# Optimization experiments

Measured on AMD Instinct MI355X. Metric: run time of the kernel, lower is better.

## Reference

```python
import jax, jax.numpy as jnp
import numpy as np

N_SA_ITERS = 3
MESH_LR = 5.0
MESH_ITERS = 4
SH_ITERS = 5
EPS = 1e-8
B, N, D, S, H = 16, 16384, 64, 7, 128


def layer_norm(x, g, b):
    m = jnp.mean(x, -1, keepdims=True)
    v = jnp.var(x, -1, keepdims=True)
    return (x - m) * jax.lax.rsqrt(v + 1e-5) * g + b


def cdist(k, q):
    # k: [b,n,d], q: [b,s,d] -> euclidean distances [b,n,s]
    k2 = jnp.sum(k * k, -1)[:, :, None]
    q2 = jnp.sum(q * q, -1)[:, None, :]
    sq = k2 + q2 - 2.0 * jnp.einsum('bnd,bsd->bns', k, q)
    return jnp.sqrt(jnp.maximum(sq, 0.0) + 1e-12)


def sinkhorn(C, log_a, log_b, u, v, n_iters=SH_ITERS):
    # log-domain Sinkhorn. C: [b,n,s], log_a: [b,n], log_b: [b,s]
    p = -C
    for _ in range(n_iters):
        u = log_a - jax.nn.logsumexp(p + v[:, None, :], axis=2)
        v = log_b - jax.nn.logsumexp(p + u[:, :, None], axis=1)
    T = jnp.exp(p + u[:, :, None] + v[:, None, :])
    return T, u, v


def minimize_entropy_of_sinkhorn(C, log_a, log_b, mesh_lr=MESH_LR, n_mesh_iters=MESH_ITERS):
    # MESH: gradient descent on transport-plan entropy wrt the cost matrix,
    # warm-starting the sinkhorn duals across mesh iterations.
    u = jnp.zeros_like(log_a)
    v = jnp.zeros_like(log_b)
    for _ in range(n_mesh_iters):
        def ent(Cc, uu, vv):
            T, u2, v2 = sinkhorn(Cc, log_a, log_b, uu, vv)
            e = -jnp.sum(T * jnp.log(T + EPS))
            return e, (u2, v2)
        (_, (u, v)), g = jax.value_and_grad(ent, has_aux=True)(
            C, jax.lax.stop_gradient(u), jax.lax.stop_gradient(v))
        C = C - mesh_lr * g
    return C, u, v


def gru_cell(x, h, W_ih, W_hh, b_ih, b_hh):
    # PyTorch nn.GRUCell semantics
    gi = x @ W_ih.T + b_ih
    gh = h @ W_hh.T + b_hh
    i_r, i_z, i_n = jnp.split(gi, 3, axis=-1)
    h_r, h_z, h_n = jnp.split(gh, 3, axis=-1)
    r = jax.nn.sigmoid(i_r + h_r)
    z = jax.nn.sigmoid(i_z + h_z)
    n = jnp.tanh(i_n + r * h_n)
    return (1.0 - z) * n + z * h


def setup_inputs() -> dict:
    key = jax.random.key(0)
    ks = jax.random.split(key, 24)
    w = lambda k, shape, s=0.05: (jax.random.normal(k, shape, dtype=jnp.float32) * s)
    return {
        'inputs': jax.random.normal(ks[0], (B, N, D), dtype=jnp.float32),
        'slots_init': jax.random.normal(ks[1], (B, S, D), dtype=jnp.float32),
        'slots_mu': w(ks[2], (1, 1, D), 0.1),
        'slots_log_sigma': w(ks[3], (1, 1, D), 0.1),
        'Wq': w(ks[4], (D, D)), 'Wk': w(ks[5], (D, D)), 'Wv': w(ks[6], (D, D)),
        'gru_Wih': w(ks[7], (3 * D, D)), 'gru_Whh': w(ks[8], (3 * D, D)),
        'gru_bih': jnp.zeros((3 * D,), jnp.float32), 'gru_bhh': jnp.zeros((3 * D,), jnp.float32),
        'fc1_W': w(ks[9], (H, D)), 'fc1_b': jnp.zeros((H,), jnp.float32),
        'fc2_W': w(ks[10], (D, H)), 'fc2_b': jnp.zeros((D,), jnp.float32),
        'ln_in_g': jnp.ones((D,), jnp.float32), 'ln_in_b': jnp.zeros((D,), jnp.float32),
        'ln_sl_g': jnp.ones((D,), jnp.float32), 'ln_sl_b': jnp.zeros((D,), jnp.float32),
        'ln_ff_g': jnp.ones((D,), jnp.float32), 'ln_ff_b': jnp.zeros((D,), jnp.float32),
        'wi_W': w(ks[11], (1, D)), 'wi_b': jnp.zeros((1,), jnp.float32),
        'ws_W': w(ks[12], (1, D)), 'ws_b': jnp.zeros((1,), jnp.float32),
    }


def reference(inputs, slots_init, slots_mu, slots_log_sigma, Wq, Wk, Wv,
              gru_Wih, gru_Whh, gru_bih, gru_bhh, fc1_W, fc1_b, fc2_W, fc2_b,
              ln_in_g, ln_in_b, ln_sl_g, ln_sl_b, ln_ff_g, ln_ff_b,
              wi_W, wi_b, ws_W, ws_b):
    b_s, n_in, d = inputs.shape
    n_s = slots_init.shape[1]
    slots = slots_mu + jnp.exp(slots_log_sigma) * slots_init
    x = layer_norm(inputs, ln_in_g, ln_in_b)
    k = x @ Wk.T
    v = x @ Wv.T
    # input marginal a (sums to n_s over the n_in axis)
    a = jax.nn.softmax((x @ wi_W.T + wi_b)[..., 0], axis=-1) * n_s
    log_a = jnp.log(a)
    attn = None
    for _ in range(N_SA_ITERS):
        slots_prev = slots
        s_n = layer_norm(slots, ln_sl_g, ln_sl_b)
        b_marg = jax.nn.softmax((s_n @ ws_W.T + ws_b)[..., 0], axis=-1) * n_s
        log_b = jnp.log(b_marg)
        q = s_n @ Wq.T
        C = cdist(k, q)                                   # [b, n_in, n_s]
        C, p_u, q_v = minimize_entropy_of_sinkhorn(C, log_a, log_b)
        attn, _, _ = sinkhorn(C, log_a, log_b, p_u, q_v)  # [b, n_in, n_s]
        attn = jnp.transpose(attn, (0, 2, 1))             # [b, n_s, n_in]
        updates = jnp.matmul(attn, v)                     # [b, n_s, d]
        slots = gru_cell(updates.reshape(b_s * n_s, d), slots_prev.reshape(b_s * n_s, d),
                         gru_Wih, gru_Whh, gru_bih, gru_bhh).reshape(b_s, n_s, d)
        ff = jax.nn.relu(layer_norm(slots, ln_ff_g, ln_ff_b) @ fc1_W.T + fc1_b) @ fc2_W.T + fc2_b
        slots = slots + ff
    return slots, attn
```

## Files before the change

### kernel.cpp

```cpp
#include <hip/hip_runtime.h>
#include <math.h>

#define AGENTS __HIP_MEMORY_SCOPE_AGENT
typedef unsigned long long u64x;

constexpr int   CB   = 16;
constexpr int   CN   = 16384;
constexpr float LOG7 = 1.9459101090932196f;
constexpr float EPST = 1e-8f;

constexpr size_t ST1 = 0;
constexpr size_t ST2 = 1024;
constexpr size_t ST3 = 5120;
constexpr size_t NST = 234496;

constexpr size_t OFF_WQT = 468992;
constexpr size_t OFF_WIH = 473088;
constexpr size_t OFF_WHH = 485376;
constexpr size_t OFF_F1T = 497664;
constexpr size_t OFF_F2T = 505856;
constexpr size_t OFF_K   = 514048;
constexpr size_t OFF_V   = OFF_K + (size_t)CB * CN * 64;

__device__ __forceinline__ u64x pkf(float v, unsigned e) {
  return ((u64x)e << 32) | (u64x)__float_as_uint(v);
}
__device__ __forceinline__ void st_rlx(u64x* p, u64x v) {
  __hip_atomic_store(p, v, __ATOMIC_RELAXED, AGENTS);
}
__device__ __forceinline__ u64x ld_rlx(const u64x* p) {
  return __hip_atomic_load(const_cast<u64x*>(p), __ATOMIC_RELAXED, AGENTS);
}
__device__ __forceinline__ float poll_f(const u64x* p, unsigned e) {
  u64x q;
  do { q = ld_rlx(p); } while ((unsigned)(q >> 32) != e);
  return __uint_as_float((unsigned)q);
}
__device__ __forceinline__ float wsum64(float v) {
#pragma unroll
  for (int m = 1; m < 64; m <<= 1) v += __shfl_xor(v, m, 64);
  return v;
}
__device__ __forceinline__ float dot4(float4 a, float4 b) {
  return a.x * b.x + a.y * b.y + a.z * b.z + a.w * b.w;
}

__global__ void prep_kernel(const float* __restrict__ Wq, const float* __restrict__ Wih,
                            const float* __restrict__ Whh, const float* __restrict__ f1,
                            const float* __restrict__ f2, float* __restrict__ w) {
  size_t idx = blockIdx.x * blockDim.x + threadIdx.x;
  size_t stride = (size_t)gridDim.x * blockDim.x;
  u64x* st = reinterpret_cast<u64x*>(w);
  for (size_t i = idx; i < NST; i += stride) st_rlx(st + i, 0ULL);
  for (size_t i = idx; i < 64 * 64; i += stride) {
    int d = i / 64, j = i % 64;
    w[OFF_WQT + j * 64 + d] = Wq[d * 64 + j];
  }
  for (size_t i = idx; i < 192 * 64; i += stride) {
    int o = i / 64, j = i % 64;
    w[OFF_WIH + j * 192 + o] = Wih[o * 64 + j];
    w[OFF_WHH + j * 192 + o] = Whh[o * 64 + j];
  }
  for (size_t i = idx; i < 128 * 64; i += stride) {
    int o = i / 64, j = i % 64;
    w[OFF_F1T + j * 128 + o] = f1[o * 64 + j];
  }
  for (size_t i = idx; i < 64 * 128; i += stride) {
    int d = i / 128, j = i % 128;
    w[OFF_F2T + j * 64 + d] = f2[d * 128 + j];
  }
}

__launch_bounds__(1024, 4)
__global__ void slot_attn_kernel(
    const float* __restrict__ inputs, const float* __restrict__ sinit,
    const float* __restrict__ smu, const float* __restrict__ slsig,
    const float* __restrict__ Wk, const float* __restrict__ Wv,
    const float* __restrict__ gbih, const float* __restrict__ gbhh,
    const float* __restrict__ fc1b, const float* __restrict__ fc2b,
    const float* __restrict__ lin_g, const float* __restrict__ lin_b,
    const float* __restrict__ lsl_g, const float* __restrict__ lsl_b,
    const float* __restrict__ lff_g, const float* __restrict__ lff_b,
    const float* __restrict__ wi_W, const float* __restrict__ wi_b,
    const float* __restrict__ wsW, const float* __restrict__ wsB,
    float* __restrict__ out, float* __restrict__ w) {
  __shared__ float s_slots[448];
  __shared__ float s_snl[448];
  __shared__ float s_q[448];
  __shared__ float s_scr1[1344];
  __shared__ float s_scr2[1344];
  __shared__ float s_updl[448];
  __shared__ float s_T[8192];
  __shared__ float s_pupd[7168];
  __shared__ float s_z[48];
  __shared__ float s_eb[8];
  __shared__ float s_rb[8];
  __shared__ float s_gvl[8];
  __shared__ float s_q2[8];
  __shared__ float s_wl[8];
  __shared__ float s_redw[128];
  __shared__ float s_gath[128];
  __shared__ float s_misc[4];

  const int tid = threadIdx.x;
  const int lane = tid & 63, wid = tid >> 6;
  const int bb = blockIdx.x & 15;
  const int ib16 = blockIdx.x >> 4;
  const size_t grow = (size_t)bb * CN + ib16 * 1024 + tid;
  u64x* st = reinterpret_cast<u64x*>(w);
  float lg;

  {
    const float* xin = inputs + grow * 64;
    float4 xa[16];
#pragma unroll
    for (int c = 0; c < 16; ++c) xa[c] = reinterpret_cast<const float4*>(xin)[c];
    float s1 = 0;
#pragma unroll
    for (int c = 0; c < 16; ++c) s1 += xa[c].x + xa[c].y + xa[c].z + xa[c].w;
    float mn = s1 * (1.f / 64.f);
    float s2 = 0;
#pragma unroll
    for (int c = 0; c < 16; ++c) {
      float dx = xa[c].x - mn, dy = xa[c].y - mn, dz = xa[c].z - mn, dw = xa[c].w - mn;
      s2 += dx * dx + dy * dy + dz * dz + dw * dw;
    }
    float rs = rsqrtf(s2 * (1.f / 64.f) + 1e-5f);
#pragma unroll
    for (int c = 0; c < 16; ++c) {
      float4 g4 = reinterpret_cast<const float4*>(lin_g)[c];
      float4 b4 = reinterpret_cast<const float4*>(lin_b)[c];
      xa[c].x = (xa[c].x - mn) * rs * g4.x + b4.x;
      xa[c].y = (xa[c].y - mn) * rs * g4.y + b4.y;
      xa[c].z = (xa[c].z - mn) * rs * g4.z + b4.z;
      xa[c].w = (xa[c].w - mn) * rs * g4.w + b4.w;
    }
    lg = wi_b[0];
#pragma unroll
    for (int c = 0; c < 16; ++c) lg += dot4(xa[c], reinterpret_cast<const float4*>(wi_W)[c]);
#pragma unroll 1
    for (int half = 0; half < 2; ++half) {
      const float* W = half ? Wv : Wk;
      float* ob = w + (half ? OFF_V : OFF_K) + grow * 64;
#pragma unroll 1
      for (int oc = 0; oc < 8; ++oc) {
        float acc[8] = {0, 0, 0, 0, 0, 0, 0, 0};
#pragma unroll
        for (int c = 0; c < 16; ++c) {
          float4 xv = xa[c];
#pragma unroll
          for (int o8 = 0; o8 < 8; ++o8) {
            float4 w4 = reinterpret_cast<const float4*>(W + (size_t)(oc * 8 + o8) * 64)[c];
            acc[o8] += dot4(xv, w4);
          }
        }
        reinterpret_cast<float4*>(ob + oc * 8)[0] = make_float4(acc[0], acc[1], acc[2], acc[3]);
        reinterpret_cast<float4*>(ob + oc * 8)[1] = make_float4(acc[4], acc[5], acc[6], acc[7]);
      }
    }
    float mx = lg;
#pragma unroll
    for (int m = 1; m < 64; m <<= 1) mx = fmaxf(mx, __shfl_xor(mx, m, 64));
    float se = wsum64(__expf(lg - mx));
    if (lane == 0) { s_redw[wid * 8 + 0] = mx; s_redw[wid * 8 + 1] = se; }
    __syncthreads();
    if (wid == 0) {
      float m0 = (lane < 16) ? s_redw[lane * 8 + 0] : -1e30f;
      float e0 = (lane < 16) ? s_redw[lane * 8 + 1] : 0.f;
#pragma unroll
      for (int mm = 1; mm < 16; mm <<= 1) {
        float m1 = __shfl_xor(m0, mm, 64), e1 = __shfl_xor(e0, mm, 64);
        float nm = fmaxf(m0, m1);
        e0 = e0 * __expf(m0 - nm) + e1 * __expf(m1 - nm);
        m0 = nm;
      }
      if (lane == 0) {
        u64x* sp = st + ST1 + (size_t)(bb * 16 + ib16) * 4;
        st_rlx(sp + 0, pkf(m0, 1u));
        st_rlx(sp + 1, pkf(e0, 1u));
      }
    }
  }

  if (wid == 0) {
    int j = lane >> 2, f = lane & 3;
    if (f < 2) {
      s_gath[j * 4 + f] = poll_f(st + ST1 + (size_t)(bb * 16 + j) * 4 + f, 1u);
    }
  }
  __syncthreads();
  if (tid == 0) {
    float m = s_gath[0], se = s_gath[1];
#pragma unroll 1
    for (int j = 1; j < 16; ++j) {
      float mj = s_gath[j * 4], ej = s_gath[j * 4 + 1];
      float nm = fmaxf(m, mj);
      se = se * __expf(m - nm) + ej * __expf(mj - nm);
      m = nm;
    }
    s_misc[0] = m + __logf(se);
  }
  __syncthreads();
  const float aval = 7.f * __expf(lg - s_misc[0]);

  unsigned e = 2;
  float p[7], E[7], eu = 0.f;

  auto exchange = [&](float (&es)[7], float* dst, bool div_eb) {
#pragma unroll
    for (int m = 1; m < 64; m <<= 1) {
#pragma unroll
      for (int s = 0; s < 7; ++s) es[s] += __shfl_xor(es[s], m, 64);
    }
    if (lane == 0) {
#pragma unroll
      for (int s = 0; s < 7; ++s) s_redw[wid * 8 + s] = es[s];
    }
    __syncthreads();
    const unsigned par = e & 1;
    u64x* base = st + ST2 + ((size_t)(bb * 2 + par) * 16) * 8;
    if (wid == 0 && lane < 7) {
      float bp = 0.f;
#pragma unroll
      for (int j = 0; j < 16; ++j) bp += s_redw[j * 8 + lane];
      st_rlx(base + (size_t)ib16 * 8 + lane, pkf(bp, e));
    }
    if (wid < 2) {
      int g = wid * 64 + lane;
      int j = g >> 3, s2 = g & 7;
      if (s2 < 7) s_gath[j * 8 + s2] = poll_f(base + (size_t)j * 8 + s2, e);
    }
    __syncthreads();
    if (tid < 7) {
      float tot = 0.f;
#pragma unroll
      for (int j = 0; j < 16; ++j) tot += s_gath[j * 8 + tid];
      dst[tid] = div_eb ? (s_eb[tid] / tot) : tot;
    }
    __syncthreads();
    ++e;
  };

  auto fwd5 = [&]() {
#pragma unroll 1
    for (int i = 1; i <= 5; ++i) {
      float t = 0.f;
#pragma unroll
      for (int s = 0; s < 7; ++s) t += E[s] * s_z[(i - 1) * 8 + s];
      eu = aval / t;
      float es[7];
#pragma unroll
      for (int s = 0; s < 7; ++s) es[s] = E[s] * eu;
      exchange(es, &s_z[i * 8], true);
    }
  };

  auto slot_common = [&]() {
    if (wid < 7) {
      float h = s_slots[wid * 64 + lane];
      float m = wsum64(h) * (1.f / 64.f);
      float d0 = h - m;
      float va = wsum64(d0 * d0) * (1.f / 64.f);
      float sn = d0 * rsqrtf(va + 1e-5f) * lsl_g[lane] + lsl_b[lane];
      s_snl[wid * 64 + lane] = sn;
      float pw = wsum64(sn * wsW[lane]);
      if (lane == 0) s_wl[wid] = pw + wsB[0];
    }
    __syncthreads();
    if (tid < 448) {
      int s = tid >> 6, dd = tid & 63;
      float acc = 0;
#pragma unroll 4
      for (int j = 0; j < 64; ++j) acc += s_snl[s * 64 + j] * w[OFF_WQT + j * 64 + dd];
      s_q[s * 64 + dd] = acc;
    }
    __syncthreads();
    if (wid < 7) {
      float qv = s_q[wid * 64 + lane];
      float q2 = wsum64(qv * qv);
      if (lane == 0) s_q2[wid] = q2;
    }
    if (tid == 0) {
      float mx = -1e30f;
#pragma unroll
      for (int s = 0; s < 7; ++s) mx = fmaxf(mx, s_wl[s]);
      float se = 0;
#pragma unroll
      for (int s = 0; s < 7; ++s) se += __expf(s_wl[s] - mx);
      float lse = mx + __logf(se);
#pragma unroll
      for (int s = 0; s < 7; ++s) {
        float ebv = __expf(s_wl[s] - lse + LOG7);
        s_eb[s] = ebv;
        s_rb[s] = 1.f / ebv;
      }
    }
    __syncthreads();
  };

  if (tid < 448) {
    int dd = tid & 63;
    s_slots[tid] = smu[dd] + __expf(slsig[dd]) * sinit[(size_t)bb * 448 + tid];
  }
  __syncthreads();
  slot_common();

#pragma unroll 1
  for (int it = 0; it < 3; ++it) {
    {
      const float* kb = w + OFF_K + grow * 64;
      float4 ka[16];
#pragma unroll
      for (int c = 0; c < 16; ++c) ka[c] = reinterpret_cast<const float4*>(kb)[c];
      float k2 = 0;
#pragma unroll
      for (int c = 0; c < 16; ++c) k2 += dot4(ka[c], ka[c]);
#pragma unroll
      for (int s = 0; s < 7; ++s) {
        float kq = 0;
#pragma unroll
        for (int c = 0; c < 16; ++c)
          kq += dot4(ka[c], *reinterpret_cast<const float4*>(&s_q[s * 64 + c * 4]));
        float sq = k2 + s_q2[s] - 2.f * kq;
        p[s] = -sqrtf(fmaxf(sq, 0.f) + 1e-12f);
        E[s] = __expf(p[s]);
      }
    }
    if (tid < 8) s_z[tid] = 1.f;
    __syncthreads();

#pragma unroll 1
    for (int ms = 0; ms < 4; ++ms) {
      fwd5();
      float gp[7], guT = 0.f;
      {
        float es[7];
#pragma unroll
        for (int s = 0; s < 7; ++s) {
          float T = E[s] * eu * s_z[40 + s];
          float gT = -(__logf(T + EPST) + T / (T + EPST));
          float g = gT * T;
          gp[s] = g; guT += g; es[s] = g;
        }
        exchange(es, s_gvl, false);
      }
#pragma unroll 1
      for (int i = 5; i >= 1; --i) {
        float t = 0.f;
#pragma unroll
        for (int s = 0; s < 7; ++s) t += E[s] * s_z[(i - 1) * 8 + s];
        float rt = 1.f / t;
        float eui = aval * rt;
        float gu = (i == 5) ? guT : 0.f;
#pragma unroll
        for (int s = 0; s < 7; ++s) {
          float sn = E[s] * eui * s_z[i * 8 + s] * s_rb[s];
          float gz = -s_gvl[s] * sn;
          gp[s] += gz; gu += gz;
        }
        float gw[7];
#pragma unroll
        for (int s = 0; s < 7; ++s) {
          float sg = E[s] * s_z[(i - 1) * 8 + s] * rt;
          gw[s] = -gu * sg;
          gp[s] += gw[s];
        }
        if (i > 1) exchange(gw, s_gvl, false);
      }
#pragma unroll
      for (int s = 0; s < 7; ++s) {
        p[s] -= 5.0f * gp[s];
        E[s] = __expf(p[s]);
      }
      if (tid < 8) s_z[tid] = s_z[40 + tid];
      __syncthreads();
    }

    fwd5();
    float T7[7];
#pragma unroll
    for (int s = 0; s < 7; ++s) T7[s] = E[s] * eu * s_z[40 + s];
    if (it == 2) {
      size_t ab = 7168 + (size_t)(bb * 7) * CN + ib16 * 1024 + tid;
#pragma unroll
      for (int s = 0; s < 7; ++s) out[ab + (size_t)s * CN] = T7[s];
    }
#pragma unroll
    for (int s = 0; s < 7; ++s) s_T[tid * 8 + s] = T7[s];
    __syncthreads();

    {
      const float* vb = w + OFF_V + (grow - tid + wid * 64) * 64 + lane;
      float acc[7] = {0, 0, 0, 0, 0, 0, 0};
#pragma unroll 4
      for (int n = 0; n < 64; ++n) {
        float vv = vb[(size_t)n * 64];
        const float* tr = &s_T[(wid * 64 + n) * 8];
        acc[0] += tr[0] * vv; acc[1] += tr[1] * vv; acc[2] += tr[2] * vv;
        acc[3] += tr[3] * vv; acc[4] += tr[4] * vv; acc[5] += tr[5] * vv;
        acc[6] += tr[6] * vv;
      }
#pragma unroll
      for (int s = 0; s < 7; ++s) s_pupd[(wid * 7 + s) * 64 + lane] = acc[s];
    }
    __syncthreads();
    {
      const unsigned par = e & 1;
      u64x* b3 = st + ST3 + ((size_t)(bb * 2 + par) * 16) * 448;
      if (tid < 448) {
        float t = 0;
#pragma unroll
        for (int w16 = 0; w16 < 16; ++w16) t += s_pupd[w16 * 448 + tid];
        st_rlx(b3 + (size_t)ib16 * 448 + tid, pkf(t, e));
        float tot; bool ok;
        do {
          tot = 0.f; ok = true;
#pragma unroll
          for (int j = 0; j < 16; ++j) {
            u64x q = ld_rlx(b3 + (size_t)j * 448 + tid);
            ok = ok && ((unsigned)(q >> 32) == e);
            tot += __uint_as_float((unsigned)q);
          }
        } while (!ok);
        s_updl[tid] = tot;
      }
      __syncthreads();
      ++e;
    }

    {
#pragma unroll 1
      for (int idx = tid; idx < 1344; idx += 1024) {
        int s = idx / 192, o = idx - s * 192;
        float g1 = gbih[o], g2 = gbhh[o];
#pragma unroll 4
        for (int j = 0; j < 64; ++j) {
          g1 += s_updl[s * 64 + j] * w[OFF_WIH + j * 192 + o];
          g2 += s_slots[s * 64 + j] * w[OFF_WHH + j * 192 + o];
        }
        s_scr1[s * 192 + o] = g1;
        s_scr2[s * 192 + o] = g2;
      }
      __syncthreads();
      if (tid < 448) {
        int s = tid >> 6, dd = tid & 63;
        float ir = s_scr1[s * 192 + dd],        hr = s_scr2[s * 192 + dd];
        float iz = s_scr1[s * 192 + 64 + dd],   hz = s_scr2[s * 192 + 64 + dd];
        float in_ = s_scr1[s * 192 + 128 + dd], hn = s_scr2[s * 192 + 128 + dd];
        float r = 1.f / (1.f + __expf(-(ir + hr)));
        float z = 1.f / (1.f + __expf(-(iz + hz)));
        float nn = tanhf(in_ + r * hn);
        s_updl[s * 64 + dd] = (1.f - z) * nn + z * s_slots[s * 64 + dd];
      }
      __syncthreads();
      if (wid < 7) {
        float h = s_updl[wid * 64 + lane];
        float m = wsum64(h) * (1.f / 64.f);
        float d0 = h - m;
        float va = wsum64(d0 * d0) * (1.f / 64.f);
        s_snl[wid * 64 + lane] = d0 * rsqrtf(va + 1e-5f) * lff_g[lane] + lff_b[lane];
      }
      __syncthreads();
      if (tid < 896) {
        int s = tid >> 7, i2 = tid & 127;
        float a1 = fc1b[i2];
#pragma unroll 4
        for (int j = 0; j < 64; ++j) a1 += s_snl[s * 64 + j] * w[OFF_F1T + j * 128 + i2];
        s_scr1[s * 128 + i2] = fmaxf(a1, 0.f);
      }
      __syncthreads();
      if (tid < 448) {
        int s = tid >> 6, dd = tid & 63;
        float a2 = fc2b[dd];
#pragma unroll 4
        for (int i2 = 0; i2 < 128; ++i2) a2 += s_scr1[s * 128 + i2] * w[OFF_F2T + i2 * 64 + dd];
        s_slots[s * 64 + dd] = s_updl[s * 64 + dd] + a2;
      }
      __syncthreads();
    }
    if (it < 2) slot_common();
  }

  if (ib16 == 0 && tid < 448) out[(size_t)bb * 448 + tid] = s_slots[tid];
}

extern "C" void kernel_launch(void* const* d_in, const int* in_sizes, int n_in,
                              void* d_out, int out_size, void* d_ws, size_t ws_size,
                              hipStream_t stream) {
  (void)in_sizes; (void)n_in; (void)out_size; (void)ws_size;
  const float* inputs = (const float*)d_in[0];
  const float* sinit  = (const float*)d_in[1];
  const float* smu    = (const float*)d_in[2];
  const float* slsig  = (const float*)d_in[3];
  const float* Wq     = (const float*)d_in[4];
  const float* Wk     = (const float*)d_in[5];
  const float* Wv     = (const float*)d_in[6];
  const float* gWih   = (const float*)d_in[7];
  const float* gWhh   = (const float*)d_in[8];
  const float* gbih   = (const float*)d_in[9];
  const float* gbhh   = (const float*)d_in[10];
  const float* fc1W   = (const float*)d_in[11];
  const float* fc1b   = (const float*)d_in[12];
  const float* fc2W   = (const float*)d_in[13];
  const float* fc2b   = (const float*)d_in[14];
  const float* ling   = (const float*)d_in[15];
  const float* linb   = (const float*)d_in[16];
  const float* lslg   = (const float*)d_in[17];
  const float* lslb   = (const float*)d_in[18];
  const float* lffg   = (const float*)d_in[19];
  const float* lffb   = (const float*)d_in[20];
  const float* wiW    = (const float*)d_in[21];
  const float* wib    = (const float*)d_in[22];
  const float* wsW    = (const float*)d_in[23];
  const float* wsb    = (const float*)d_in[24];
  float* out = (float*)d_out;
  float* w   = (float*)d_ws;

  prep_kernel<<<dim3(64), dim3(256), 0, stream>>>(Wq, gWih, gWhh, fc1W, fc2W, w);
  slot_attn_kernel<<<dim3(256), dim3(1024), 0, stream>>>(
      inputs, sinit, smu, slsig, Wk, Wv, gbih, gbhh, fc1b, fc2b,
      ling, linb, lslg, lslb, lffg, lffb, wiW, wib, wsW, wsb, out, w);
}
```

Before: 1.755 ms.

## Collapse per-batch work onto one block, spilling cost and gradient planes to global memory

After the projection phase, only 16 blocks (one per batch) continue. Each block loops over all 16 row chunks, staging cost logits and gradients in workspace buffers instead of registers. This removes every cross-block flag exchange in the Sinkhorn, MESH backward and update reductions, replacing them with block-local reductions. The trade-off is far less parallelism (16 blocks on a large GPU) and repeated global traffic plus exp recomputation each pass. It also adds a fast reciprocal and sleep-based polling.

```diff
diff --git a/kernel.cpp b/kernel.cpp
--- a/kernel.cpp
+++ b/kernel.cpp
@@ -10,17 +10,18 @@
 constexpr float EPST = 1e-8f;
 
 constexpr size_t ST1 = 0;
-constexpr size_t ST2 = 1024;
-constexpr size_t ST3 = 5120;
-constexpr size_t NST = 234496;
-
-constexpr size_t OFF_WQT = 468992;
-constexpr size_t OFF_WIH = 473088;
-constexpr size_t OFF_WHH = 485376;
-constexpr size_t OFF_F1T = 497664;
-constexpr size_t OFF_F2T = 505856;
-constexpr size_t OFF_K   = 514048;
-constexpr size_t OFF_V   = OFF_K + (size_t)CB * CN * 64;
+constexpr size_t NST = 512;
+
+constexpr size_t OFF_LG  = 1024;
+constexpr size_t OFF_P   = 263168;
+constexpr size_t OFF_PN  = 2360320;
+constexpr size_t OFF_WQT = 4457472;
+constexpr size_t OFF_WIH = 4461568;
+constexpr size_t OFF_WHH = 4473856;
+constexpr size_t OFF_F1T = 4486144;
+constexpr size_t OFF_F2T = 4494336;
+constexpr size_t OFF_K   = 4502528;
+constexpr size_t OFF_V   = 21279744;
 
 __device__ __forceinline__ u64x pkf(float v, unsigned e) {
   return ((u64x)e << 32) | (u64x)__float_as_uint(v);
@@ -31,10 +32,16 @@
 __device__ __forceinline__ u64x ld_rlx(const u64x* p) {
   return __hip_atomic_load(const_cast<u64x*>(p), __ATOMIC_RELAXED, AGENTS);
 }
-__device__ __forceinline__ float poll_f(const u64x* p, unsigned e) {
+__device__ __forceinline__ float poll_sc1(const u64x* p, unsigned e) {
   u64x q;
-  do { q = ld_rlx(p); } while ((unsigned)(q >> 32) != e);
+  do {
+    q = ld_rlx(p);
+    if ((unsigned)(q >> 32) != e) __builtin_amdgcn_s_sleep(2);
+  } while ((unsigned)(q >> 32) != e);
   return __uint_as_float((unsigned)q);
+}
+__device__ __forceinline__ float frcp(float x) {
+  float r; asm("v_rcp_f32 %0, %1" : "=v"(r) : "v"(x)); return r;
 }
 __device__ __forceinline__ float wsum64(float v) {
 #pragma unroll
@@ -99,18 +106,17 @@
   __shared__ float s_q2[8];
   __shared__ float s_wl[8];
   __shared__ float s_redw[128];
-  __shared__ float s_gath[128];
+  __shared__ float s_gath[32];
   __shared__ float s_misc[4];
 
   const int tid = threadIdx.x;
   const int lane = tid & 63, wid = tid >> 6;
   const int bb = blockIdx.x & 15;
   const int ib16 = blockIdx.x >> 4;
-  const size_t grow = (size_t)bb * CN + ib16 * 1024 + tid;
   u64x* st = reinterpret_cast<u64x*>(w);
-  float lg;
 
   {
+    const size_t grow = (size_t)bb * CN + (size_t)ib16 * 1024 + tid;
     const float* xin = inputs + grow * 64;
     float4 xa[16];
 #pragma unroll
@@ -135,9 +141,10 @@
       xa[c].z = (xa[c].z - mn) * rs * g4.z + b4.z;
       xa[c].w = (xa[c].w - mn) * rs * g4.w + b4.w;
     }
-    lg = wi_b[0];
+    float lg = wi_b[0];
 #pragma unroll
     for (int c = 0; c < 16; ++c) lg += dot4(xa[c], reinterpret_cast<const float4*>(wi_W)[c]);
+    w[OFF_LG + grow] = lg;
 #pragma unroll 1
     for (int half = 0; half < 2; ++half) {
       const float* W = half ? Wv : Wk;
@@ -163,8 +170,10 @@
     for (int m = 1; m < 64; m <<= 1) mx = fmaxf(mx, __shfl_xor(mx, m, 64));
     float se = wsum64(__expf(lg - mx));
     if (lane == 0) { s_redw[wid * 8 + 0] = mx; s_redw[wid * 8 + 1] = se; }
+    asm volatile("s_waitcnt vmcnt(0)" ::: "memory");
     __syncthreads();
     if (wid == 0) {
+      __threadfence();
       float m0 = (lane < 16) ? s_redw[lane * 8 + 0] : -1e30f;
       float e0 = (lane < 16) ? s_redw[lane * 8 + 1] : 0.f;
 #pragma unroll
@@ -175,25 +184,25 @@
         m0 = nm;
       }
       if (lane == 0) {
-        u64x* sp = st + ST1 + (size_t)(bb * 16 + ib16) * 4;
+        u64x* sp = st + ST1 + (size_t)(bb * 16 + ib16) * 2;
         st_rlx(sp + 0, pkf(m0, 1u));
         st_rlx(sp + 1, pkf(e0, 1u));
       }
     }
   }
 
-  if (wid == 0) {
-    int j = lane >> 2, f = lane & 3;
-    if (f < 2) {
-      s_gath[j * 4 + f] = poll_f(st + ST1 + (size_t)(bb * 16 + j) * 4 + f, 1u);
-    }
+  if (blockIdx.x >= 16) return;
+
+  if (wid == 0 && lane < 32) {
+    int j = lane >> 1, f = lane & 1;
+    s_gath[lane] = poll_sc1(st + ST1 + (size_t)(bb * 16 + j) * 2 + f, 1u);
   }
   __syncthreads();
   if (tid == 0) {
     float m = s_gath[0], se = s_gath[1];
 #pragma unroll 1
     for (int j = 1; j < 16; ++j) {
-      float mj = s_gath[j * 4], ej = s_gath[j * 4 + 1];
+      float mj = s_gath[j * 2], ej = s_gath[j * 2 + 1];
       float nm = fmaxf(m, mj);
       se = se * __expf(m - nm) + ej * __expf(mj - nm);
       m = nm;
@@ -201,12 +210,14 @@
     s_misc[0] = m + __logf(se);
   }
   __syncthreads();
-  const float aval = 7.f * __expf(lg - s_misc[0]);
-
-  unsigned e = 2;
-  float p[7], E[7], eu = 0.f;
-
-  auto exchange = [&](float (&es)[7], float* dst, bool div_eb) {
+  const float lseA = s_misc[0];
+  __threadfence();
+  __syncthreads();
+
+  float* P = w + OFF_P  + (size_t)bb * CN * 8;
+  float* G = w + OFF_PN + (size_t)bb * CN * 8;
+
+  auto red7 = [&](float (&es)[7], float* dst, bool div_eb) {
 #pragma unroll
     for (int m = 1; m < 64; m <<= 1) {
 #pragma unroll
@@ -217,41 +228,35 @@
       for (int s = 0; s < 7; ++s) s_redw[wid * 8 + s] = es[s];
     }
     __syncthreads();
-    const unsigned par = e & 1;
-    u64x* base = st + ST2 + ((size_t)(bb * 2 + par) * 16) * 8;
     if (wid == 0 && lane < 7) {
-      float bp = 0.f;
-#pragma unroll
-      for (int j = 0; j < 16; ++j) bp += s_redw[j * 8 + lane];
-      st_rlx(base + (size_t)ib16 * 8 + lane, pkf(bp, e));
-    }
-    if (wid < 2) {
-      int g = wid * 64 + lane;
-      int j = g >> 3, s2 = g & 7;
-      if (s2 < 7) s_gath[j * 8 + s2] = poll_f(base + (size_t)j * 8 + s2, e);
-    }
-    __syncthreads();
-    if (tid < 7) {
       float tot = 0.f;
 #pragma unroll
-      for (int j = 0; j < 16; ++j) tot += s_gath[j * 8 + tid];
-      dst[tid] = div_eb ? (s_eb[tid] / tot) : tot;
-    }
-    __syncthreads();
-    ++e;
+      for (int j = 0; j < 16; ++j) tot += s_redw[j * 8 + lane];
+      dst[lane] = div_eb ? (s_eb[lane] / tot) : tot;
+    }
+    __syncthreads();
   };
 
   auto fwd5 = [&]() {
 #pragma unroll 1
     for (int i = 1; i <= 5; ++i) {
-      float t = 0.f;
-#pragma unroll
-      for (int s = 0; s < 7; ++s) t += E[s] * s_z[(i - 1) * 8 + s];
-      eu = aval / t;
-      float es[7];
-#pragma unroll
-      for (int s = 0; s < 7; ++s) es[s] = E[s] * eu;
-      exchange(es, &s_z[i * 8], true);
+      float z0 = s_z[(i - 1) * 8 + 0], z1 = s_z[(i - 1) * 8 + 1], z2 = s_z[(i - 1) * 8 + 2],
+            z3 = s_z[(i - 1) * 8 + 3], z4 = s_z[(i - 1) * 8 + 4], z5 = s_z[(i - 1) * 8 + 5],
+            z6 = s_z[(i - 1) * 8 + 6];
+      float es[7] = {0, 0, 0, 0, 0, 0, 0};
+#pragma unroll 2
+      for (int r = 0; r < 16; ++r) {
+        const float* pr = P + ((size_t)r * 1024 + tid) * 8;
+        float4 pa = *reinterpret_cast<const float4*>(pr);
+        float4 pb = *reinterpret_cast<const float4*>(pr + 4);
+        float E0 = __expf(pa.x), E1 = __expf(pa.y), E2 = __expf(pa.z), E3 = __expf(pa.w);
+        float E4 = __expf(pb.x), E5 = __expf(pb.y), E6 = __expf(pb.z);
+        float t = E0 * z0 + E1 * z1 + E2 * z2 + E3 * z3 + E4 * z4 + E5 * z5 + E6 * z6;
+        float eu = pb.w * frcp(t);
+        es[0] += E0 * eu; es[1] += E1 * eu; es[2] += E2 * eu; es[3] += E3 * eu;
+        es[4] += E4 * eu; es[5] += E5 * eu; es[6] += E6 * eu;
+      }
+      red7(es, &s_z[i * 8], true);
     }
   };
 
@@ -307,24 +312,34 @@
 
 #pragma unroll 1
   for (int it = 0; it < 3; ++it) {
-    {
-      const float* kb = w + OFF_K + grow * 64;
-      float4 ka[16];
-#pragma unroll
-      for (int c = 0; c < 16; ++c) ka[c] = reinterpret_cast<const float4*>(kb)[c];
-      float k2 = 0;
-#pragma unroll
-      for (int c = 0; c < 16; ++c) k2 += dot4(ka[c], ka[c]);
-#pragma unroll
-      for (int s = 0; s < 7; ++s) {
-        float kq = 0;
-#pragma unroll
-        for (int c = 0; c < 16; ++c)
-          kq += dot4(ka[c], *reinterpret_cast<const float4*>(&s_q[s * 64 + c * 4]));
-        float sq = k2 + s_q2[s] - 2.f * kq;
-        p[s] = -sqrtf(fmaxf(sq, 0.f) + 1e-12f);
-        E[s] = __expf(p[s]);
-      }
+#pragma unroll 1
+    for (int r = 0; r < 16; ++r) {
+      const float* kb = w + OFF_K + ((size_t)bb * CN + (size_t)r * 1024 + tid) * 64;
+      float k2 = 0, kq0 = 0, kq1 = 0, kq2 = 0, kq3 = 0, kq4 = 0, kq5 = 0, kq6 = 0;
+#pragma unroll 4
+      for (int c = 0; c < 16; ++c) {
+        float4 kk = *reinterpret_cast<const float4*>(kb + c * 4);
+        k2  += dot4(kk, kk);
+        kq0 += dot4(kk, *reinterpret_cast<const float4*>(&s_q[0 * 64 + c * 4]));
+        kq1 += dot4(kk, *reinterpret_cast<const float4*>(&s_q[1 * 64 + c * 4]));
+        kq2 += dot4(kk, *reinterpret_cast<const float4*>(&s_q[2 * 64 + c * 4]));
+        kq3 += dot4(kk, *reinterpret_cast<const float4*>(&s_q[3 * 64 + c * 4]));
+        kq4 += dot4(kk, *reinterpret_cast<const float4*>(&s_q[4 * 64 + c * 4]));
+        kq5 += dot4(kk, *reinterpret_cast<const float4*>(&s_q[5 * 64 + c * 4]));
+        kq6 += dot4(kk, *reinterpret_cast<const float4*>(&s_q[6 * 64 + c * 4]));
+      }
+      float p0 = -sqrtf(fmaxf(k2 + s_q2[0] - 2.f * kq0, 0.f) + 1e-12f);
+      float p1 = -sqrtf(fmaxf(k2 + s_q2[1] - 2.f * kq1, 0.f) + 1e-12f);
+      float p2 = -sqrtf(fmaxf(k2 + s_q2[2] - 2.f * kq2, 0.f) + 1e-12f);
+      float p3 = -sqrtf(fmaxf(k2 + s_q2[3] - 2.f * kq3, 0.f) + 1e-12f);
+      float p4 = -sqrtf(fmaxf(k2 + s_q2[4] - 2.f * kq4, 0.f) + 1e-12f);
+      float p5 = -sqrtf(fmaxf(k2 + s_q2[5] - 2.f * kq5, 0.f) + 1e-12f);
+      float p6 = -sqrtf(fmaxf(k2 + s_q2[6] - 2.f * kq6, 0.f) + 1e-12f);
+      float lgr = w[OFF_LG + (size_t)bb * CN + (size_t)r * 1024 + tid];
+      float av = 7.f * __expf(lgr - lseA);
+      float* pw = P + ((size_t)r * 1024 + tid) * 8;
+      *reinterpret_cast<float4*>(pw)     = make_float4(p0, p1, p2, p3);
+      *reinterpret_cast<float4*>(pw + 4) = make_float4(p4, p5, p6, av);
     }
     if (tid < 8) s_z[tid] = 1.f;
     __syncthreads();
@@ -332,100 +347,151 @@
 #pragma unroll 1
     for (int ms = 0; ms < 4; ++ms) {
       fwd5();
-      float gp[7], guT = 0.f;
       {
-        float es[7];
-#pragma unroll
-        for (int s = 0; s < 7; ++s) {
-          float T = E[s] * eu * s_z[40 + s];
-          float gT = -(__logf(T + EPST) + T / (T + EPST));
-          float g = gT * T;
-          gp[s] = g; guT += g; es[s] = g;
+        float zm0 = s_z[32], zm1 = s_z[33], zm2 = s_z[34], zm3 = s_z[35],
+              zm4 = s_z[36], zm5 = s_z[37], zm6 = s_z[38];
+        float zf0 = s_z[40], zf1 = s_z[41], zf2 = s_z[42], zf3 = s_z[43],
+              zf4 = s_z[44], zf5 = s_z[45], zf6 = s_z[46];
+        float es[7] = {0, 0, 0, 0, 0, 0, 0};
+#pragma unroll 2
+        for (int r = 0; r < 16; ++r) {
+          const float* pr = P + ((size_t)r * 1024 + tid) * 8;
+          float4 pa = *reinterpret_cast<const float4*>(pr);
+          float4 pb = *reinterpret_cast<const float4*>(pr + 4);
+          float E0 = __expf(pa.x), E1 = __expf(pa.y), E2 = __expf(pa.z), E3 = __expf(pa.w);
+          float E4 = __expf(pb.x), E5 = __expf(pb.y), E6 = __expf(pb.z);
+          float t = E0 * zm0 + E1 * zm1 + E2 * zm2 + E3 * zm3 + E4 * zm4 + E5 * zm5 + E6 * zm6;
+          float eu = pb.w * frcp(t);
+          float T0 = E0 * eu * zf0, T1 = E1 * eu * zf1, T2 = E2 * eu * zf2,
+                T3 = E3 * eu * zf3, T4 = E4 * eu * zf4, T5 = E5 * eu * zf5, T6 = E6 * eu * zf6;
+          float g0 = -(__logf(T0 + EPST) + T0 * frcp(T0 + EPST)) * T0;
+          float g1 = -(__logf(T1 + EPST) + T1 * frcp(T1 + EPST)) * T1;
+          float g2 = -(__logf(T2 + EPST) + T2 * frcp(T2 + EPST)) * T2;
+          float g3 = -(__logf(T3 + EPST) + T3 * frcp(T3 + EPST)) * T3;
+          float g4 = -(__logf(T4 + EPST) + T4 * frcp(T4 + EPST)) * T4;
+          float g5 = -(__logf(T5 + EPST) + T5 * frcp(T5 + EPST)) * T5;
+          float g6 = -(__logf(T6 + EPST) + T6 * frcp(T6 + EPST)) * T6;
+          float gs = g0 + g1 + g2 + g3 + g4 + g5 + g6;
+          float* gr = G + ((size_t)r * 1024 + tid) * 8;
+          *reinterpret_cast<float4*>(gr)     = make_float4(g0, g1, g2, g3);
+          *reinterpret_cast<float4*>(gr + 4) = make_float4(g4, g5, g6, gs);
+          es[0] += g0; es[1] += g1; es[2] += g2; es[3] += g3;
+          es[4] += g4; es[5] += g5; es[6] += g6;
         }
-        exchange(es, s_gvl, false);
+        red7(es, s_gvl, false);
       }
 #pragma unroll 1
       for (int i = 5; i >= 1; --i) {
-        float t = 0.f;
-#pragma unroll
-        for (int s = 0; s < 7; ++s) t += E[s] * s_z[(i - 1) * 8 + s];
-        float rt = 1.f / t;
-        float eui = aval * rt;
-        float gu = (i == 5) ? guT : 0.f;
-#pragma unroll
-        for (int s = 0; s < 7; ++s) {
-          float sn = E[s] * eui * s_z[i * 8 + s] * s_rb[s];
-          float gz = -s_gvl[s] * sn;
-          gp[s] += gz; gu += gz;
+        float zm0 = s_z[(i - 1) * 8 + 0], zm1 = s_z[(i - 1) * 8 + 1], zm2 = s_z[(i - 1) * 8 + 2],
+              zm3 = s_z[(i - 1) * 8 + 3], zm4 = s_z[(i - 1) * 8 + 4], zm5 = s_z[(i - 1) * 8 + 5],
+              zm6 = s_z[(i - 1) * 8 + 6];
+        float w0 = s_z[i * 8 + 0] * s_rb[0] * s_gvl[0], w1 = s_z[i * 8 + 1] * s_rb[1] * s_gvl[1],
+              w2 = s_z[i * 8 + 2] * s_rb[2] * s_gvl[2], w3 = s_z[i * 8 + 3] * s_rb[3] * s_gvl[3],
+              w4 = s_z[i * 8 + 4] * s_rb[4] * s_gvl[4], w5 = s_z[i * 8 + 5] * s_rb[5] * s_gvl[5],
+              w6 = s_z[i * 8 + 6] * s_rb[6] * s_gvl[6];
+        float es[7] = {0, 0, 0, 0, 0, 0, 0};
+#pragma unroll 2
+        for (int r = 0; r < 16; ++r) {
+          float* pr = P + ((size_t)r * 1024 + tid) * 8;
+          float* gr = G + ((size_t)r * 1024 + tid) * 8;
+          float4 pa = *reinterpret_cast<const float4*>(pr);
+          float4 pb = *reinterpret_cast<const float4*>(pr + 4);
+          float4 ga = *reinterpret_cast<const float4*>(gr);
+          float4 gb = *reinterpret_cast<const float4*>(gr + 4);
+          float E0 = __expf(pa.x), E1 = __expf(pa.y), E2 = __expf(pa.z), E3 = __expf(pa.w);
+          float E4 = __expf(pb.x), E5 = __expf(pb.y), E6 = __expf(pb.z);
+          float t = E0 * zm0 + E1 * zm1 + E2 * zm2 + E3 * zm3 + E4 * zm4 + E5 * zm5 + E6 * zm6;
+          float rt = frcp(t);
+          float eui = pb.w * rt;
+          float gu = (i == 5) ? gb.w : 0.f;
+          float gz0 = -w0 * E0 * eui; gu += gz0;
+          float gz1 = -w1 * E1 * eui; gu += gz1;
+          float gz2 = -w2 * E2 * eui; gu += gz2;
+          float gz3 = -w3 * E3 * eui; gu += gz3;
+          float gz4 = -w4 * E4 * eui; gu += gz4;
+          float gz5 = -w5 * E5 * eui; gu += gz5;
+          float gz6 = -w6 * E6 * eui; gu += gz6;
+          float a0 = ga.x + gz0, a1 = ga.y + gz1, a2 = ga.z + gz2, a3 = ga.w + gz3;
+          float a4 = gb.x + gz4, a5 = gb.y + gz5, a6 = gb.z + gz6;
+          float c = gu * rt;
+          float gw0 = -c * E0 * zm0; a0 += gw0; es[0] += gw0;
+          float gw1 = -c * E1 * zm1; a1 += gw1; es[1] += gw1;
+          float gw2 = -c * E2 * zm2; a2 += gw2; es[2] += gw2;
+          float gw3 = -c * E3 * zm3; a3 += gw3; es[3] += gw3;
+          float gw4 = -c * E4 * zm4; a4 += gw4; es[4] += gw4;
+          float gw5 = -c * E5 * zm5; a5 += gw5; es[5] += gw5;
+          float gw6 = -c * E6 * zm6; a6 += gw6; es[6] += gw6;
+          if (i > 1) {
+            *reinterpret_cast<float4*>(gr)     = make_float4(a0, a1, a2, a3);
+            *reinterpret_cast<float4*>(gr + 4) = make_float4(a4, a5, a6, 0.f);
+          } else {
+            *reinterpret_cast<float4*>(pr) =
+                make_float4(pa.x - 5.f * a0, pa.y - 5.f * a1, pa.z - 5.f * a2, pa.w - 5.f * a3);
+            *reinterpret_cast<float4*>(pr + 4) =
+                make_float4(pb.x - 5.f * a4, pb.y - 5.f * a5, pb.z - 5.f * a6, pb.w);
+          }
         }
-        float gw[7];
-#pragma unroll
-        for (int s = 0; s < 7; ++s) {
-          float sg = E[s] * s_z[(i - 1) * 8 + s] * rt;
-          gw[s] = -gu * sg;
-          gp[s] += gw[s];
+        if (i > 1) red7(es, s_gvl, false);
+      }
+      if (tid < 7) s_z[tid] = s_z[40 + tid];
+      __syncthreads();
+    }
+
+    fwd5();
+
+    {
+      float zm0 = s_z[32], zm1 = s_z[33], zm2 = s_z[34], zm3 = s_z[35],
+            zm4 = s_z[36], zm5 = s_z[37], zm6 = s_z[38];
+      float zf0 = s_z[40], zf1 = s_z[41], zf2 = s_z[42], zf3 = s_z[43],
+            zf4 = s_z[44], zf5 = s_z[45], zf6 = s_z[46];
+      float ac0 = 0, ac1 = 0, ac2 = 0, ac3 = 0, ac4 = 0, ac5 = 0, ac6 = 0;
+#pragma unroll 1
+      for (int pass = 0; pass < 16; ++pass) {
+        const float* pr = P + ((size_t)pass * 1024 + tid) * 8;
+        float4 pa = *reinterpret_cast<const float4*>(pr);
+        float4 pb = *reinterpret_cast<const float4*>(pr + 4);
+        float E0 = __expf(pa.x), E1 = __expf(pa.y), E2 = __expf(pa.z), E3 = __expf(pa.w);
+        float E4 = __expf(pb.x), E5 = __expf(pb.y), E6 = __expf(pb.z);
+        float t = E0 * zm0 + E1 * zm1 + E2 * zm2 + E3 * zm3 + E4 * zm4 + E5 * zm5 + E6 * zm6;
+        float eu = pb.w * frcp(t);
+        float T0 = E0 * eu * zf0, T1 = E1 * eu * zf1, T2 = E2 * eu * zf2,
+              T3 = E3 * eu * zf3, T4 = E4 * eu * zf4, T5 = E5 * eu * zf5, T6 = E6 * eu * zf6;
+        if (it == 2) {
+          size_t rowg = (size_t)pass * 1024 + tid;
+          size_t ab = 7168 + (size_t)(bb * 7) * CN + rowg;
+          out[ab] = T0; out[ab + (size_t)CN] = T1; out[ab + (size_t)2 * CN] = T2;
+          out[ab + (size_t)3 * CN] = T3; out[ab + (size_t)4 * CN] = T4;
+          out[ab + (size_t)5 * CN] = T5; out[ab + (size_t)6 * CN] = T6;
         }
-        if (i > 1) exchange(gw, s_gvl, false);
-      }
-#pragma unroll
-      for (int s = 0; s < 7; ++s) {
-        p[s] -= 5.0f * gp[s];
-        E[s] = __expf(p[s]);
-      }
-      if (tid < 8) s_z[tid] = s_z[40 + tid];
-      __syncthreads();
-    }
-
-    fwd5();
-    float T7[7];
-#pragma unroll
-    for (int s = 0; s < 7; ++s) T7[s] = E[s] * eu * s_z[40 + s];
-    if (it == 2) {
-      size_t ab = 7168 + (size_t)(bb * 7) * CN + ib16 * 1024 + tid;
-#pragma unroll
-      for (int s = 0; s < 7; ++s) out[ab + (size_t)s * CN] = T7[s];
-    }
-#pragma unroll
-    for (int s = 0; s < 7; ++s) s_T[tid * 8 + s] = T7[s];
-    __syncthreads();
-
-    {
-      const float* vb = w + OFF_V + (grow - tid + wid * 64) * 64 + lane;
-      float acc[7] = {0, 0, 0, 0, 0, 0, 0};
+        float* tr = &s_T[tid * 8];
+        tr[0] = T0; tr[1] = T1; tr[2] = T2; tr[3] = T3; tr[4] = T4; tr[5] = T5; tr[6] = T6;
+        __syncthreads();
+        const float* vb = w + OFF_V +
+            ((size_t)bb * CN + (size_t)pass * 1024 + wid * 64) * 64 + lane;
 #pragma unroll 4
-      for (int n = 0; n < 64; ++n) {
-        float vv = vb[(size_t)n * 64];
-        const float* tr = &s_T[(wid * 64 + n) * 8];
-        acc[0] += tr[0] * vv; acc[1] += tr[1] * vv; acc[2] += tr[2] * vv;
-        acc[3] += tr[3] * vv; acc[4] += tr[4] * vv; acc[5] += tr[5] * vv;
-        acc[6] += tr[6] * vv;
-      }
-#pragma unroll
-      for (int s = 0; s < 7; ++s) s_pupd[(wid * 7 + s) * 64 + lane] = acc[s];
-    }
-    __syncthreads();
-    {
-      const unsigned par = e & 1;
-      u64x* b3 = st + ST3 + ((size_t)(bb * 2 + par) * 16) * 448;
+        for (int n = 0; n < 64; ++n) {
+          float vv = __builtin_nontemporal_load(vb + (size_t)n * 64);
+          const float* tq = &s_T[(wid * 64 + n) * 8];
+          ac0 += tq[0] * vv; ac1 += tq[1] * vv; ac2 += tq[2] * vv;
+          ac3 += tq[3] * vv; ac4 += tq[4] * vv; ac5 += tq[5] * vv; ac6 += tq[6] * vv;
+        }
+        __syncthreads();
+      }
+      s_pupd[(wid * 7 + 0) * 64 + lane] = ac0;
+      s_pupd[(wid * 7 + 1) * 64 + lane] = ac1;
+      s_pupd[(wid * 7 + 2) * 64 + lane] = ac2;
+      s_pupd[(wid * 7 + 3) * 64 + lane] = ac3;
+      s_pupd[(wid * 7 + 4) * 64 + lane] = ac4;
+      s_pupd[(wid * 7 + 5) * 64 + lane] = ac5;
+      s_pupd[(wid * 7 + 6) * 64 + lane] = ac6;
+      __syncthreads();
       if (tid < 448) {
         float t = 0;
 #pragma unroll
         for (int w16 = 0; w16 < 16; ++w16) t += s_pupd[w16 * 448 + tid];
-        st_rlx(b3 + (size_t)ib16 * 448 + tid, pkf(t, e));
-        float tot; bool ok;
-        do {
-          tot = 0.f; ok = true;
-#pragma unroll
-          for (int j = 0; j < 16; ++j) {
-            u64x q = ld_rlx(b3 + (size_t)j * 448 + tid);
-            ok = ok && ((unsigned)(q >> 32) == e);
-            tot += __uint_as_float((unsigned)q);
-          }
-        } while (!ok);
-        s_updl[tid] = tot;
-      }
-      __syncthreads();
-      ++e;
+        s_updl[tid] = t;
+      }
+      __syncthreads();
     }
 
     {
@@ -448,9 +514,9 @@
         float iz = s_scr1[s * 192 + 64 + dd],   hz = s_scr2[s * 192 + 64 + dd];
         float in_ = s_scr1[s * 192 + 128 + dd], hn = s_scr2[s * 192 + 128 + dd];
         float r = 1.f / (1.f + __expf(-(ir + hr)));
-        float z = 1.f / (1.f + __expf(-(iz + hz)));
+        float zz = 1.f / (1.f + __expf(-(iz + hz)));
         float nn = tanhf(in_ + r * hn);
-        s_updl[s * 64 + dd] = (1.f - z) * nn + z * s_slots[s * 64 + dd];
+        s_updl[s * 64 + dd] = (1.f - zz) * nn + zz * s_slots[s * 64 + dd];
       }
       __syncthreads();
       if (wid < 7) {
@@ -481,7 +547,10 @@
     if (it < 2) slot_common();
   }
 
-  if (ib16 == 0 && tid < 448) out[(size_t)bb * 448 + tid] = s_slots[tid];
+  if (tid < 448) out[(size_t)bb * 448 + tid] = s_slots[tid];
+
+  __syncthreads();
+  if (wid == 0) __threadfence();
 }
 
 extern "C" void kernel_launch(void* const* d_in, const int* in_sizes, int n_in,
```

Measured after the change: 3.665 ms. +108.9%, slower.

## Replace per-step backward Sinkhorn exchanges with one batched Jacobian reduction

Applied to the files above, without the earlier changes.

The backward pass through the five Sinkhorn steps used to need a grid-wide exchange for every step. Each block now reduces all the per-step 7x7 Jacobian terms and the initial gradient vectors into one 210-float buffer. A single cross-block all-reduce shares it, and thread 0 then runs the backward chain for the v-gradients locally. This removes several global barrier round-trips per mesh iteration, at the cost of more wave reductions, a larger shared-memory footprint and serial work on one thread. Polling loops also gain s_sleep backoff to reduce memory contention while spinning.

```diff
diff --git a/kernel.cpp b/kernel.cpp
--- a/kernel.cpp
+++ b/kernel.cpp
@@ -10,17 +10,18 @@
 constexpr float EPST = 1e-8f;
 
 constexpr size_t ST1 = 0;
-constexpr size_t ST2 = 1024;
-constexpr size_t ST3 = 5120;
-constexpr size_t NST = 234496;
-
-constexpr size_t OFF_WQT = 468992;
-constexpr size_t OFF_WIH = 473088;
-constexpr size_t OFF_WHH = 485376;
-constexpr size_t OFF_F1T = 497664;
-constexpr size_t OFF_F2T = 505856;
-constexpr size_t OFF_K   = 514048;
-constexpr size_t OFF_V   = OFF_K + (size_t)CB * CN * 64;
+constexpr size_t ST2 = 512;
+constexpr size_t ST3 = 4608;
+constexpr size_t ST4 = 233984;
+constexpr size_t NST = 365056;
+
+constexpr size_t OFF_WQT = 730112;
+constexpr size_t OFF_WIH = 734208;
+constexpr size_t OFF_WHH = 746496;
+constexpr size_t OFF_F1T = 758784;
+constexpr size_t OFF_F2T = 766976;
+constexpr size_t OFF_K   = 775168;
+constexpr size_t OFF_V   = 17552384;
 
 __device__ __forceinline__ u64x pkf(float v, unsigned e) {
   return ((u64x)e << 32) | (u64x)__float_as_uint(v);
@@ -31,9 +32,12 @@
 __device__ __forceinline__ u64x ld_rlx(const u64x* p) {
   return __hip_atomic_load(const_cast<u64x*>(p), __ATOMIC_RELAXED, AGENTS);
 }
-__device__ __forceinline__ float poll_f(const u64x* p, unsigned e) {
+__device__ __forceinline__ float poll_sc1(const u64x* p, unsigned e) {
   u64x q;
-  do { q = ld_rlx(p); } while ((unsigned)(q >> 32) != e);
+  do {
+    q = ld_rlx(p);
+    if ((unsigned)(q >> 32) != e) __builtin_amdgcn_s_sleep(2);
+  } while ((unsigned)(q >> 32) != e);
   return __uint_as_float((unsigned)q);
 }
 __device__ __forceinline__ float wsum64(float v) {
@@ -95,18 +99,20 @@
   __shared__ float s_z[48];
   __shared__ float s_eb[8];
   __shared__ float s_rb[8];
-  __shared__ float s_gvl[8];
   __shared__ float s_q2[8];
   __shared__ float s_wl[8];
   __shared__ float s_redw[128];
   __shared__ float s_gath[128];
+  __shared__ float s_mw[3360];
+  __shared__ float s_M[216];
+  __shared__ float s_gva[48];
   __shared__ float s_misc[4];
 
   const int tid = threadIdx.x;
   const int lane = tid & 63, wid = tid >> 6;
   const int bb = blockIdx.x & 15;
   const int ib16 = blockIdx.x >> 4;
-  const size_t grow = (size_t)bb * CN + ib16 * 1024 + tid;
+  const size_t grow = (size_t)bb * CN + (size_t)ib16 * 1024 + tid;
   u64x* st = reinterpret_cast<u64x*>(w);
   float lg;
 
@@ -163,6 +169,7 @@
     for (int m = 1; m < 64; m <<= 1) mx = fmaxf(mx, __shfl_xor(mx, m, 64));
     float se = wsum64(__expf(lg - mx));
     if (lane == 0) { s_redw[wid * 8 + 0] = mx; s_redw[wid * 8 + 1] = se; }
+    asm volatile("s_waitcnt vmcnt(0)" ::: "memory");
     __syncthreads();
     if (wid == 0) {
       float m0 = (lane < 16) ? s_redw[lane * 8 + 0] : -1e30f;
@@ -175,7 +182,7 @@
         m0 = nm;
       }
       if (lane == 0) {
-        u64x* sp = st + ST1 + (size_t)(bb * 16 + ib16) * 4;
+        u64x* sp = st + ST1 + (size_t)(bb * 16 + ib16) * 2;
         st_rlx(sp + 0, pkf(m0, 1u));
         st_rlx(sp + 1, pkf(e0, 1u));
       }
@@ -185,7 +192,7 @@
   if (wid == 0) {
     int j = lane >> 2, f = lane & 3;
     if (f < 2) {
-      s_gath[j * 4 + f] = poll_f(st + ST1 + (size_t)(bb * 16 + j) * 4 + f, 1u);
+      s_gath[j * 4 + f] = poll_sc1(st + ST1 + (size_t)(bb * 16 + j) * 2 + f, 1u);
     }
   }
   __syncthreads();
@@ -217,8 +224,7 @@
       for (int s = 0; s < 7; ++s) s_redw[wid * 8 + s] = es[s];
     }
     __syncthreads();
-    const unsigned par = e & 1;
-    u64x* base = st + ST2 + ((size_t)(bb * 2 + par) * 16) * 8;
+    u64x* base = st + ST2 + ((size_t)(bb * 2 + (e & 1)) * 16) * 8;
     if (wid == 0 && lane < 7) {
       float bp = 0.f;
 #pragma unroll
@@ -228,7 +234,7 @@
     if (wid < 2) {
       int g = wid * 64 + lane;
       int j = g >> 3, s2 = g & 7;
-      if (s2 < 7) s_gath[j * 8 + s2] = poll_f(base + (size_t)j * 8 + s2, e);
+      if (s2 < 7) s_gath[j * 8 + s2] = poll_sc1(base + (size_t)j * 8 + s2, e);
     }
     __syncthreads();
     if (tid < 7) {
@@ -252,6 +258,16 @@
 #pragma unroll
       for (int s = 0; s < 7; ++s) es[s] = E[s] * eu;
       exchange(es, &s_z[i * 8], true);
+    }
+  };
+
+  auto wred = [&](const float* v, int n, int off) {
+#pragma unroll 1
+    for (int k = 0; k < n; ++k) {
+      float x = v[k];
+#pragma unroll
+      for (int m = 1; m < 64; m <<= 1) x += __shfl_xor(x, m, 64);
+      if (lane == 0) s_mw[wid * 210 + off + k] = x;
     }
   };
 
@@ -332,46 +348,125 @@
 #pragma unroll 1
     for (int ms = 0; ms < 4; ++ms) {
       fwd5();
-      float gp[7], guT = 0.f;
+      float g7[7], gTs = 0.f;
       {
-        float es[7];
+        float t5 = 0.f;
+#pragma unroll
+        for (int s = 0; s < 7; ++s) t5 += E[s] * s_z[32 + s];
+        float rt5 = 1.f / t5, eu5 = aval * rt5;
+        float va[14];
 #pragma unroll
         for (int s = 0; s < 7; ++s) {
-          float T = E[s] * eu * s_z[40 + s];
-          float gT = -(__logf(T + EPST) + T / (T + EPST));
-          float g = gT * T;
-          gp[s] = g; guT += g; es[s] = g;
-        }
-        exchange(es, s_gvl, false);
-      }
-#pragma unroll 1
-      for (int i = 5; i >= 1; --i) {
-        float t = 0.f;
-#pragma unroll
-        for (int s = 0; s < 7; ++s) t += E[s] * s_z[(i - 1) * 8 + s];
-        float rt = 1.f / t;
-        float eui = aval * rt;
-        float gu = (i == 5) ? guT : 0.f;
+          float T = E[s] * eu5 * s_z[40 + s];
+          float gg = -(__logf(T + EPST) + T / (T + EPST)) * T;
+          g7[s] = gg; gTs += gg;
+          va[s] = gg;
+        }
+#pragma unroll
+        for (int s = 0; s < 7; ++s)
+          va[7 + s] = gTs * (E[s] * s_z[32 + s] * rt5);
+        wred(va, 14, 0);
+#pragma unroll 1
+        for (int i = 5; i >= 2; --i) {
+          float t = 0.f;
+#pragma unroll
+          for (int s = 0; s < 7; ++s) t += E[s] * s_z[(i - 1) * 8 + s];
+          float rt = 1.f / t, eui = aval * rt;
+          float sn[7], sg[7];
+#pragma unroll
+          for (int s = 0; s < 7; ++s) {
+            sn[s] = E[s] * eui * s_z[i * 8 + s] * s_rb[s];
+            sg[s] = E[s] * s_z[(i - 1) * 8 + s] * rt;
+          }
+          int off = 14 + (5 - i) * 49;
+          float vb[28];
+#pragma unroll
+          for (int s = 0; s < 4; ++s)
+#pragma unroll
+            for (int s2 = 0; s2 < 7; ++s2) vb[s * 7 + s2] = sn[s2] * sg[s];
+          wred(vb, 28, off);
+          float vc[21];
+#pragma unroll
+          for (int s = 4; s < 7; ++s)
+#pragma unroll
+            for (int s2 = 0; s2 < 7; ++s2) vc[(s - 4) * 7 + s2] = sn[s2] * sg[s];
+          wred(vc, 21, off + 28);
+        }
+      }
+      __syncthreads();
+      {
+        u64x* b4 = st + ST4 + ((size_t)(bb * 2 + (e & 1)) * 16) * 256;
+        if (tid < 210) {
+          float t = 0.f;
+#pragma unroll
+          for (int j = 0; j < 16; ++j) t += s_mw[j * 210 + tid];
+          st_rlx(b4 + (size_t)ib16 * 256 + tid, pkf(t, e));
+          float tot; bool ok;
+          do {
+            tot = 0.f; ok = true;
+#pragma unroll
+            for (int j = 0; j < 16; ++j) {
+              u64x q = ld_rlx(b4 + (size_t)j * 256 + tid);
+              ok = ok && ((unsigned)(q >> 32) == e);
+              tot += __uint_as_float((unsigned)q);
+            }
+            if (!ok) __builtin_amdgcn_s_sleep(1);
+          } while (!ok);
+          s_M[tid] = tot;
+        }
+        __syncthreads();
+        ++e;
+      }
+      if (tid == 0) {
+        float gv[7];
+#pragma unroll
+        for (int s = 0; s < 7; ++s) { gv[s] = s_M[s]; s_gva[40 + s] = gv[s]; }
+#pragma unroll 1
+        for (int i = 5; i >= 2; --i) {
+          float nv[7];
+#pragma unroll
+          for (int s = 0; s < 7; ++s) {
+            float acc = (i == 5) ? -s_M[7 + s] : 0.f;
+#pragma unroll
+            for (int s2 = 0; s2 < 7; ++s2)
+              acc += s_M[14 + (5 - i) * 49 + s * 7 + s2] * gv[s2];
+            nv[s] = acc;
+          }
+#pragma unroll
+          for (int s = 0; s < 7; ++s) { gv[s] = nv[s]; s_gva[(i - 1) * 8 + s] = nv[s]; }
+        }
+      }
+      __syncthreads();
+      {
+        float gp[7];
+#pragma unroll
+        for (int s = 0; s < 7; ++s) gp[s] = g7[s];
+#pragma unroll 1
+        for (int i = 5; i >= 1; --i) {
+          float t = 0.f;
+#pragma unroll
+          for (int s = 0; s < 7; ++s) t += E[s] * s_z[(i - 1) * 8 + s];
+          float rt = 1.f / t, eui = aval * rt;
+          float gu = (i == 5) ? gTs : 0.f;
+#pragma unroll
+          for (int s = 0; s < 7; ++s) {
+            float sn = E[s] * eui * s_z[i * 8 + s] * s_rb[s];
+            float gz = -s_gva[i * 8 + s] * sn;
+            gp[s] += gz; gu += gz;
+          }
+#pragma unroll
+          for (int s = 0; s < 7; ++s) {
+            float sg = E[s] * s_z[(i - 1) * 8 + s] * rt;
+            gp[s] += -gu * sg;
+          }
+        }
 #pragma unroll
         for (int s = 0; s < 7; ++s) {
-          float sn = E[s] * eui * s_z[i * 8 + s] * s_rb[s];
-          float gz = -s_gvl[s] * sn;
-          gp[s] += gz; gu += gz;
-        }
-        float gw[7];
-#pragma unroll
-        for (int s = 0; s < 7; ++s) {
-          float sg = E[s] * s_z[(i - 1) * 8 + s] * rt;
-          gw[s] = -gu * sg;
-          gp[s] += gw[s];
-        }
-        if (i > 1) exchange(gw, s_gvl, false);
-      }
-#pragma unroll
-      for (int s = 0; s < 7; ++s) {
-        p[s] -= 5.0f * gp[s];
-        E[s] = __expf(p[s]);
-      }
+          p[s] -= 5.0f * gp[s];
+          E[s] = __expf(p[s]);
+        }
+      }
+      __syncthreads();
       if (tid < 8) s_z[tid] = s_z[40 + tid];
       __syncthreads();
     }
@@ -381,7 +476,7 @@
 #pragma unroll
     for (int s = 0; s < 7; ++s) T7[s] = E[s] * eu * s_z[40 + s];
     if (it == 2) {
-      size_t ab = 7168 + (size_t)(bb * 7) * CN + ib16 * 1024 + tid;
+      size_t ab = 7168 + (size_t)(bb * 7) * CN + (size_t)ib16 * 1024 + tid;
 #pragma unroll
       for (int s = 0; s < 7; ++s) out[ab + (size_t)s * CN] = T7[s];
     }
@@ -405,8 +500,7 @@
     }
     __syncthreads();
     {
-      const unsigned par = e & 1;
-      u64x* b3 = st + ST3 + ((size_t)(bb * 2 + par) * 16) * 448;
+      u64x* b3 = st + ST3 + ((size_t)(bb * 2 + (e & 1)) * 16) * 448;
       if (tid < 448) {
         float t = 0;
 #pragma unroll
@@ -421,6 +515,7 @@
             ok = ok && ((unsigned)(q >> 32) == e);
             tot += __uint_as_float((unsigned)q);
           }
+          if (!ok) __builtin_amdgcn_s_sleep(1);
         } while (!ok);
         s_updl[tid] = tot;
       }
@@ -448,9 +543,9 @@
         float iz = s_scr1[s * 192 + 64 + dd],   hz = s_scr2[s * 192 + 64 + dd];
         float in_ = s_scr1[s * 192 + 128 + dd], hn = s_scr2[s * 192 + 128 + dd];
         float r = 1.f / (1.f + __expf(-(ir + hr)));
-        float z = 1.f / (1.f + __expf(-(iz + hz)));
+        float zz = 1.f / (1.f + __expf(-(iz + hz)));
         float nn = tanhf(in_ + r * hn);
-        s_updl[s * 64 + dd] = (1.f - z) * nn + z * s_slots[s * 64 + dd];
+        s_updl[s * 64 + dd] = (1.f - zz) * nn + zz * s_slots[s * 64 + dd];
       }
       __syncthreads();
       if (wid < 7) {
```

Result: slower. 2.600 ms (+48.2%).
